# Kernel optimization log

Measured on AMD Instinct MI355X. Metric: run time of the kernel, lower is better.

The kernel has to match this reference:

```python
import jax, jax.numpy as jnp
import numpy as np

RATIO = 2          # BigVGAN Activation1d up/down ratio
K_FILT = 12        # int(6 * ratio // 2) * 2
DILATIONS = (1, 3, 5)


def _kaiser_sinc_filter1d(cutoff, half_width, kernel_size):
    # Faithful port of BigVGAN's kaiser_sinc_filter1d (even kernel path).
    half_size = kernel_size // 2
    delta_f = 4.0 * half_width
    A = 2.285 * (half_size - 1) * np.pi * delta_f + 7.95
    if A > 50.0:
        beta = 0.1102 * (A - 8.7)
    elif A >= 21.0:
        beta = 0.5842 * (A - 21.0) ** 0.4 + 0.07886 * (A - 21.0)
    else:
        beta = 0.0
    window = np.kaiser(kernel_size, beta)              # periodic=False
    time = np.arange(-half_size, half_size) + 0.5       # even kernel size
    filt = 2.0 * cutoff * window * np.sinc(2.0 * cutoff * time)
    filt = filt / filt.sum()
    return jnp.asarray(filt, dtype=jnp.float32)

FILT = _kaiser_sinc_filter1d(0.5 / RATIO, 0.6 / RATIO, K_FILT)


def _depthwise1d(x, filt, stride, lhs_dilation, padding):
    # x: (B, T, C), filt: (k,) shared across channels (depthwise)
    C = x.shape[-1]
    kern = jnp.tile(filt[:, None, None], (1, 1, C))  # (k, 1, C)
    return jax.lax.conv_general_dilated(
        x, kern, window_strides=(stride,), padding=padding,
        lhs_dilation=(lhs_dilation,), feature_group_count=C,
        dimension_numbers=('NLC', 'LIO', 'NLC'))


def upsample2(x):
    # BigVGAN UpSample1d(ratio=2): replicate pad -> conv_transpose -> crop
    pad = K_FILT // RATIO - 1                       # 5
    pad_left = pad * RATIO + (K_FILT - RATIO) // 2  # 15
    pad_right = pad * RATIO + (K_FILT - RATIO + 1) // 2  # 15
    x = jnp.pad(x, ((0, 0), (pad, pad), (0, 0)), mode='edge')
    # conv_transpose(stride=r) == lhs-dilated conv with full padding
    # (filter is symmetric, so no flip needed)
    y = RATIO * _depthwise1d(x, FILT, 1, RATIO, [(K_FILT - 1, K_FILT - 1)])
    return y[:, pad_left:-pad_right, :]  # (B, 2T, C)


def downsample2(x):
    # BigVGAN DownSample1d(ratio=2) == LowPassFilter1d(stride=2)
    pad_left = K_FILT // 2 - 1  # 5 (even kernel)
    pad_right = K_FILT // 2     # 6
    x = jnp.pad(x, ((0, 0), (pad_left, pad_right), (0, 0)), mode='edge')
    return _depthwise1d(x, FILT, RATIO, 1, 'VALID')  # (B, T, C)


def snake(x, log_alpha):
    # alpha_logscale=True: alpha = exp(param); x + (1/alpha) sin^2(alpha x)
    alpha = jnp.exp(log_alpha)  # (C,), broadcasts over (B, T, C)
    return x + (1.0 / (alpha + 1e-9)) * jnp.square(jnp.sin(alpha * x))


def act1d(x, log_alpha):
    return downsample2(snake(upsample2(x), log_alpha))


def wn_conv(x, v, g, b, dilation):
    # weight-norm: kernel = v / ||v||_(0,1) * g, then SAME dilated conv
    norm = jnp.linalg.norm(v, axis=(0, 1))[None, None, :]  # (1,1,Cout)
    kern = (v / norm) * g  # (k, Cin, Cout)
    y = jax.lax.conv_general_dilated(
        x, kern, window_strides=(1,), padding='SAME',
        rhs_dilation=(dilation,), dimension_numbers=('NLC', 'LIO', 'NLC'))
    return y + b


def setup_inputs() -> dict:
    key = jax.random.key(0)
    ks = jax.random.split(key, 7)
    B, T, C, K = 4, 8192, 512, 3
    n = len(DILATIONS)
    x = jax.random.normal(ks[0], (B, T, C), dtype=jnp.float32)
    v1 = jax.random.normal(ks[1], (n, K, C, C), dtype=jnp.float32)
    g1 = jax.random.uniform(ks[2], (n, 1, 1, C), dtype=jnp.float32)
    b1 = 0.01 * jax.random.normal(ks[3], (n, C), dtype=jnp.float32)
    v2 = jax.random.normal(ks[4], (n, K, C, C), dtype=jnp.float32)
    g2 = jax.random.uniform(ks[5], (n, 1, 1, C), dtype=jnp.float32)
    b2 = 0.01 * jax.random.normal(ks[6], (n, C), dtype=jnp.float32)
    alphas = jnp.zeros((2 * n, C), dtype=jnp.float32)  # log-alpha init 0
    return {'x': x, 'v1': v1, 'g1': g1, 'b1': b1,
            'v2': v2, 'g2': g2, 'b2': b2, 'alphas': alphas}


def reference(x, v1, g1, b1, v2, g2, b2, alphas):
    for i, d in enumerate(DILATIONS):
        xt = act1d(x, alphas[2 * i])
        xt = wn_conv(xt, v1[i], g1[i], b1[i], d)
        xt = act1d(xt, alphas[2 * i + 1])
        xt = wn_conv(xt, v2[i], g2[i], b2[i], 1)
        x = xt + x
    return x
```

## Files before the change

kernel.cpp:

```cpp
#include <hip/hip_runtime.h>
#include <math.h>

#define TLEN   8192
#define CCH    512
#define NBATCH 4
#define GUARD_B 8
#define GUARD_T 16
#define XROWS  (TLEN + GUARD_B + GUARD_T)

typedef __attribute__((ext_vector_type(8))) short short8;
typedef __attribute__((ext_vector_type(4))) float f32x4;

struct Filt { float f[12]; };

#define MFMA16(a, b, c) __builtin_amdgcn_mfma_f32_16x16x32_bf16(a, b, c, 0, 0, 0)
#define VMCNT(n)  asm volatile("s_waitcnt vmcnt(" #n ")" ::: "memory")

__device__ __forceinline__ unsigned short f2bf(float f) {
  unsigned u = __float_as_uint(f);
  unsigned r = (u + 0x7fffu + ((u >> 16) & 1u)) >> 16;
  return (unsigned short)r;
}

__device__ __forceinline__ float bf2f(unsigned short u) {
  return __uint_as_float((unsigned)u << 16);
}

__device__ __forceinline__ float fast_sin(float x) {
  float r = x * 0.15915494309189535f;
  r -= floorf(r);
  return __builtin_amdgcn_sinf(r);
}

__device__ __forceinline__ float snake1(float u, float a, float rcp) {
  float s = fast_sin(a * u);
  return fmaf(rcp * s, s, u);
}

__device__ __forceinline__ void gload16(const void* g, void* l) {
  __builtin_amdgcn_global_load_lds(
      (const __attribute__((address_space(1))) unsigned int*)g,
      (__attribute__((address_space(3))) unsigned int*)l, 16, 0, 0);
}

__global__ __launch_bounds__(256)
void normp_k(const float* __restrict__ v1, const float* __restrict__ v2,
             float* __restrict__ part) {
  __shared__ float red[256];
  const int c  = blockIdx.x;
  const int cc = blockIdx.y;
  const int jc = blockIdx.z;
  const int col = threadIdx.x & 63;
  const int js  = threadIdx.x >> 6;
  const int co = cc * 64 + col;
  const float* v = (c < 3) ? v1 + (size_t)c * 3 * CCH * CCH
                           : v2 + (size_t)(c - 3) * 3 * CCH * CCH;
  const int j0 = jc * 64 + js * 16;
  float s = 0.f;
  #pragma unroll
  for (int jj = 0; jj < 16; ++jj) {
    float w = v[(size_t)(j0 + jj) * CCH + co];
    s = fmaf(w, w, s);
  }
  red[threadIdx.x] = s;
  __syncthreads();
  if (threadIdx.x < 64) {
    float t = red[threadIdx.x] + red[threadIdx.x + 64] +
              red[threadIdx.x + 128] + red[threadIdx.x + 192];
    part[(size_t)(c * CCH + co) * 24 + jc] = t;
  }
}

__global__ __launch_bounds__(256)
void fin_k(const float* __restrict__ part, const float* __restrict__ g1,
           const float* __restrict__ g2, float* __restrict__ scl) {
  const int i = blockIdx.x * 256 + threadIdx.x;
  const int c = i >> 9, co = i & 511;
  float s = 0.f;
  #pragma unroll
  for (int jc = 0; jc < 24; ++jc) s += part[(size_t)i * 24 + jc];
  const float g = (c < 3) ? g1[c * CCH + co] : g2[(c - 3) * CCH + co];
  scl[i] = g / sqrtf(s);
}

__global__ __launch_bounds__(512)
void zguard_k(unsigned short* __restrict__ xb) {
  const int b = blockIdx.x / 24;
  const int g = blockIdx.x % 24;
  const int row = (g < 8) ? g : (TLEN + g);
  xb[((size_t)b * XROWS + row) * CCH + threadIdx.x] = 0;
}

__global__ __launch_bounds__(256)
void wprep_k(const float* __restrict__ v1, const float* __restrict__ v2,
             const float* __restrict__ scl, unsigned short* __restrict__ wp) {
  const int gtid = blockIdx.x * 256 + threadIdx.x;
  const int lane = gtid & 63;
  const int gw = gtid >> 6;
  const int c  = gw / 1536;
  const int r  = gw - c * 1536;
  const int s  = r >> 5;
  const int r2 = r & 31;
  const int g8 = r2 >> 2;
  const int j  = r2 & 3;
  const int tap = s % 3, c16 = s / 3;
  const int co  = g8 * 64 + j * 16 + (lane & 15);
  const int ci0 = c16 * 32 + (lane >> 4) * 8;
  const float* v = (c < 3) ? v1 + (size_t)c * 3 * CCH * CCH
                           : v2 + (size_t)(c - 3) * 3 * CCH * CCH;
  const float sc = scl[c * CCH + co];
  unsigned short o[8];
  #pragma unroll
  for (int jj = 0; jj < 8; ++jj) {
    float w = v[((size_t)tap * CCH + ci0 + jj) * CCH + co] * sc;
    o[jj] = f2bf(w);
  }
  *reinterpret_cast<short8*>(wp + (size_t)gw * 512 + lane * 8) =
      *reinterpret_cast<const short8*>(o);
}

template<int INBF>
__global__ __launch_bounds__(256)
void act_k(const void* __restrict__ xin, unsigned short* __restrict__ y,
           const float* __restrict__ la, Filt F) {
  const int idx = blockIdx.x * 256 + threadIdx.x;
  const int c  = (idx & 127) << 2;
  const int ts = (idx >> 7) & 2047;
  const int b  = idx >> 18;
  const int t0 = ts * 4;

  auto ldrow = [&](int row) -> f32x4 {
    if constexpr (INBF) {
      const unsigned short* p =
          (const unsigned short*)xin + ((size_t)b * TLEN + row) * CCH + c;
      ushort4 u = *reinterpret_cast<const ushort4*>(p);
      f32x4 r;
      r[0] = bf2f(u.x); r[1] = bf2f(u.y); r[2] = bf2f(u.z); r[3] = bf2f(u.w);
      return r;
    } else {
      const float* p = (const float*)xin + ((size_t)b * TLEN + row) * CCH + c;
      return *reinterpret_cast<const f32x4*>(p);
    }
  };

  float av[4], rv[4];
  #pragma unroll
  for (int ch = 0; ch < 4; ++ch) {
    av[ch] = expf(la[c + ch]);
    rv[ch] = 1.f / (av[ch] + 1e-9f);
  }

  float acc[4][4];

  if (ts >= 2 && ts <= 2045) {
    f32x4 xw[14];
    #pragma unroll
    for (int j = 0; j < 14; ++j) xw[j] = ldrow(t0 - 5 + j);

    #pragma unroll
    for (int ch = 0; ch < 4; ++ch) {
      float s[18];
      #pragma unroll
      for (int mi = 0; mi < 18; ++mi) {
        float u = 0.f;
        if (mi & 1) {
          const int base = (mi - 5) / 2 + 2;
          #pragma unroll
          for (int r = 0; r < 6; ++r) u = fmaf(F.f[2*r], xw[base + r][ch], u);
        } else {
          const int base = (mi - 6) / 2 + 3;
          #pragma unroll
          for (int r = 0; r < 6; ++r) u = fmaf(F.f[2*r+1], xw[base + r][ch], u);
        }
        u *= 2.f;
        s[mi] = snake1(u, av[ch], rv[ch]);
      }
      #pragma unroll
      for (int tt = 0; tt < 4; ++tt) {
        float a = 0.f;
        #pragma unroll
        for (int k = 0; k < 12; ++k) a = fmaf(F.f[k], s[2*tt + k], a);
        acc[tt][ch] = a;
      }
    }
  } else {
    #pragma unroll
    for (int tt = 0; tt < 4; ++tt) {
      const int t = t0 + tt;
      float a0=0.f, a1=0.f, a2=0.f, a3=0.f;
      for (int k = 0; k < 12; ++k) {
        int m  = 2*t + k - 5;
        int mc = m < 0 ? 0 : (m > 2*TLEN - 1 ? 2*TLEN - 1 : m);
        int tp = mc >> 1;
        int odd = mc & 1;
        float u0=0.f,u1=0.f,u2=0.f,u3=0.f;
        #pragma unroll
        for (int r = 0; r < 6; ++r) {
          int i  = odd ? (tp + r - 2) : (tp + r - 3);
          int ic = i < 0 ? 0 : (i > TLEN - 1 ? TLEN - 1 : i);
          float tap = odd ? F.f[2*r+1] : F.f[2*r];
          f32x4 xv = ldrow(ic);
          u0 = fmaf(tap, xv[0], u0); u1 = fmaf(tap, xv[1], u1);
          u2 = fmaf(tap, xv[2], u2); u3 = fmaf(tap, xv[3], u3);
        }
        u0 *= 2.f; u1 *= 2.f; u2 *= 2.f; u3 *= 2.f;
        const float fk = F.f[k];
        a0 = fmaf(fk, snake1(u0,av[0],rv[0]), a0);
        a1 = fmaf(fk, snake1(u1,av[1],rv[1]), a1);
        a2 = fmaf(fk, snake1(u2,av[2],rv[2]), a2);
        a3 = fmaf(fk, snake1(u3,av[3],rv[3]), a3);
      }
      acc[tt][0]=a0; acc[tt][1]=a1; acc[tt][2]=a2; acc[tt][3]=a3;
    }
  }

  #pragma unroll
  for (int tt = 0; tt < 4; ++tt) {
    ushort4 o;
    o.x = f2bf(acc[tt][0]); o.y = f2bf(acc[tt][1]);
    o.z = f2bf(acc[tt][2]); o.w = f2bf(acc[tt][3]);
    *reinterpret_cast<ushort4*>(
        y + ((size_t)b * XROWS + GUARD_B + t0 + tt) * CCH + c) = o;
  }
}

template<int DIL, int MODE>
__global__ __launch_bounds__(256, 2)
void convm_k(const unsigned short* __restrict__ xb,
             const unsigned short* __restrict__ wp,
             const float* __restrict__ bia,
             const float* __restrict__ resf,
             const unsigned short* __restrict__ resb,
             float* __restrict__ outf,
             unsigned short* __restrict__ outb) {
  __shared__ unsigned short Abuf[4][2][140 * 32];

  const int tid  = threadIdx.x;
  const int lane = tid & 63;
  const int w    = tid >> 6;
  const int wr   = w >> 1;
  const int wc   = w & 1;

  const int l   = (blockIdx.x & 7) * 64 + (blockIdx.x >> 3);
  const int coB = l & 3;
  const int tb  = l >> 2;
  const int b   = tb >> 5;
  const int t0w = (tb & 31) * 256 + wr * 128;
  const int co0 = coB * 128 + wc * 64;
  const int g8  = coB * 2 + wc;

  const int qq = lane >> 4;
  const int r0 = lane & 15;
  const int a_r = lane >> 2;
  const int a_c = lane & 3;

  const unsigned short* xw0 =
      xb + ((size_t)b * XROWS + GUARD_B + t0w - 6) * CCH;
  unsigned short* const As0 = &Abuf[w][0][0];
  unsigned short* const As1 = &Abuf[w][1][0];

  f32x4 acc[8][4] = {};

  auto stA = [&](int c16, unsigned short* dst) {
    #pragma unroll
    for (int i = 0; i < 9; ++i) {
      const int rb = (i < 8) ? 16 * i : 124;
      const int R  = rb + a_r;
      const int sc = a_c ^ ((R >> 1) & 3);
      gload16(xw0 + (size_t)R * CCH + c16 * 32 + sc * 8, dst + rb * 32);
    }
  };

  stA(0, As0);

  for (int c16 = 0; c16 < 16; ++c16) {
    VMCNT(0);
    const unsigned short* Ab = (c16 & 1) ? As1 : As0;
    if (c16 < 15) stA(c16 + 1, (c16 & 1) ? As0 : As1);

    #pragma unroll
    for (int tap = 0; tap < 3; ++tap) {
      const int s = c16 * 3 + tap;
      const unsigned short* wb =
          wp + (((size_t)s * 8 + g8) * 4) * 512 + lane * 8;
      short8 bf[4];
      #pragma unroll
      for (int j = 0; j < 4; ++j)
        bf[j] = *reinterpret_cast<const short8*>(wb + (size_t)j * 512);

      const int rbase = 6 + (tap - 1) * DIL;
      short8 af[8];
      #pragma unroll
      for (int i = 0; i < 8; ++i) {
        const int row = rbase + i * 16 + r0;
        af[i] = *reinterpret_cast<const short8*>(
            Ab + row * 32 + (qq ^ ((row >> 1) & 3)) * 8);
      }
      __builtin_amdgcn_s_setprio(1);
      #pragma unroll
      for (int i = 0; i < 8; ++i)
        #pragma unroll
        for (int j = 0; j < 4; ++j)
          acc[i][j] = MFMA16(af[i], bf[j], acc[i][j]);
      __builtin_amdgcn_s_setprio(0);
    }
  }

  #pragma unroll
  for (int j = 0; j < 4; ++j) {
    const int co = co0 + j * 16 + r0;
    const float bv = bia[co];
    #pragma unroll
    for (int i = 0; i < 8; ++i) {
      const int t = t0w + i * 16 + qq * 4;
      #pragma unroll
      for (int e = 0; e < 4; ++e) {
        const size_t off = ((size_t)b * TLEN + t + e) * CCH + co;
        float o = acc[i][j][e] + bv;
        if constexpr (MODE == 1) o += resf[off];
        if constexpr (MODE == 2 || MODE == 3) o += bf2f(resb[off]);
        if constexpr (MODE == 3) outf[off] = o;
        else                     outb[off] = f2bf(o);
      }
    }
  }
}

static double bessel_i0(double x) {
  double t = 1.0, s = 1.0, q = x * x * 0.25;
  for (int k = 1; k < 64; ++k) {
    t *= q / ((double)k * (double)k);
    s += t;
    if (t < 1e-18 * s) break;
  }
  return s;
}

static void make_filter(Filt* F) {
  const double cutoff = 0.25, hw = 0.3;
  const int ks = 12, half = 6;
  const double A = 2.285 * (half - 1) * M_PI * (4.0 * hw) + 7.95;
  double beta;
  if (A > 50.0)       beta = 0.1102 * (A - 8.7);
  else if (A >= 21.0) beta = 0.5842 * pow(A - 21.0, 0.4) + 0.07886 * (A - 21.0);
  else                beta = 0.0;
  const double i0b = bessel_i0(beta);
  double f[12], sum = 0.0;
  for (int n = 0; n < 12; ++n) {
    double rr = 2.0 * n / (ks - 1) - 1.0;
    double w  = bessel_i0(beta * sqrt(fmax(0.0, 1.0 - rr * rr))) / i0b;
    double tm = (double)(n - half) + 0.5;
    double sx = 2.0 * cutoff * tm;
    double snc = (sx == 0.0) ? 1.0 : sin(M_PI * sx) / (M_PI * sx);
    f[n] = 2.0 * cutoff * w * snc;
    sum += f[n];
  }
  for (int n = 0; n < 12; ++n) F->f[n] = (float)(f[n] / sum);
}

extern "C" void kernel_launch(void* const* d_in, const int* in_sizes, int n_in,
                              void* d_out, int out_size, void* d_ws, size_t ws_size,
                              hipStream_t stream) {
  (void)in_sizes; (void)n_in; (void)out_size; (void)ws_size;
  const float* x  = (const float*)d_in[0];
  const float* v1 = (const float*)d_in[1];
  const float* g1 = (const float*)d_in[2];
  const float* b1 = (const float*)d_in[3];
  const float* v2 = (const float*)d_in[4];
  const float* g2 = (const float*)d_in[5];
  const float* b2 = (const float*)d_in[6];
  const float* al = (const float*)d_in[7];
  float* out = (float*)d_out;

  const size_t N = (size_t)NBATCH * TLEN * CCH;
  unsigned short* wb1  = (unsigned short*)d_ws;
  unsigned short* xbuf = wb1 + N;
  unsigned short* xres = xbuf + (size_t)NBATCH * XROWS * CCH;
  unsigned short* wp   = xres + N;
  float* part = (float*)(wp + (size_t)6 * 3 * CCH * CCH);
  float* scl  = part + (size_t)6 * CCH * 24;

  Filt F;
  make_filter(&F);

  zguard_k<<<96, 512, 0, stream>>>(xbuf);
  normp_k<<<dim3(6, 8, 24), 256, 0, stream>>>(v1, v2, part);
  fin_k<<<12, 256, 0, stream>>>(part, g1, g2, scl);
  wprep_k<<<2304, 256, 0, stream>>>(v1, v2, scl, wp);

  const int cgrid = NBATCH * (TLEN / 256) * 4;
  const int nblk_act = (NBATCH * 2048 * 128) / 256;
  const size_t wsz = (size_t)3 * CCH * CCH;

  act_k<0><<<nblk_act, 256, 0, stream>>>(x, xbuf, al + 0 * CCH, F);
  convm_k<1, 0><<<cgrid, 256, 0, stream>>>(xbuf, wp + 0 * wsz, b1 + 0 * CCH,
                                           nullptr, nullptr, nullptr, wb1);
  act_k<1><<<nblk_act, 256, 0, stream>>>(wb1, xbuf, al + 1 * CCH, F);
  convm_k<1, 1><<<cgrid, 256, 0, stream>>>(xbuf, wp + 3 * wsz, b2 + 0 * CCH,
                                           x, nullptr, nullptr, xres);

  act_k<1><<<nblk_act, 256, 0, stream>>>(xres, xbuf, al + 2 * CCH, F);
  convm_k<3, 0><<<cgrid, 256, 0, stream>>>(xbuf, wp + 1 * wsz, b1 + 1 * CCH,
                                           nullptr, nullptr, nullptr, wb1);
  act_k<1><<<nblk_act, 256, 0, stream>>>(wb1, xbuf, al + 3 * CCH, F);
  convm_k<1, 2><<<cgrid, 256, 0, stream>>>(xbuf, wp + 4 * wsz, b2 + 1 * CCH,
                                           nullptr, xres, nullptr, xres);

  act_k<1><<<nblk_act, 256, 0, stream>>>(xres, xbuf, al + 4 * CCH, F);
  convm_k<5, 0><<<cgrid, 256, 0, stream>>>(xbuf, wp + 2 * wsz, b1 + 2 * CCH,
                                           nullptr, nullptr, nullptr, wb1);
  act_k<1><<<nblk_act, 256, 0, stream>>>(wb1, xbuf, al + 5 * CCH, F);
  convm_k<1, 3><<<cgrid, 256, 0, stream>>>(xbuf, wp + 5 * wsz, b2 + 2 * CCH,
                                           nullptr, xres, out, nullptr);
}
```

Baseline: 651.6 us.

## Restructure conv GEMM to full-channel tiles with shared LDS weights and channel-blocked input

The activation buffer moves to a channel-blocked layout (16 panels of 32 channels, each time-contiguous), so one 32-channel slab of a time tile is a single contiguous load. The conv kernel now uses 512-thread blocks that each cover 128 timesteps by all 512 output channels. Weights are staged through double-buffered shared memory and shared by all waves, instead of every wave reading them straight from global memory. This reduces redundant weight and input traffic, but adds a block-wide barrier per tap step, uses more shared memory, and holds larger per-wave accumulators that may lower occupancy.

```diff
diff --git a/kernel.cpp b/kernel.cpp
--- a/kernel.cpp
+++ b/kernel.cpp
@@ -14,7 +14,6 @@
 struct Filt { float f[12]; };
 
 #define MFMA16(a, b, c) __builtin_amdgcn_mfma_f32_16x16x32_bf16(a, b, c, 0, 0, 0)
-#define VMCNT(n)  asm volatile("s_waitcnt vmcnt(" #n ")" ::: "memory")
 
 __device__ __forceinline__ unsigned short f2bf(float f) {
   unsigned u = __float_as_uint(f);
@@ -88,7 +87,9 @@
   const int b = blockIdx.x / 24;
   const int g = blockIdx.x % 24;
   const int row = (g < 8) ? g : (TLEN + g);
-  xb[((size_t)b * XROWS + row) * CCH + threadIdx.x] = 0;
+  const int cb = threadIdx.x >> 5;
+  const int ci = threadIdx.x & 31;
+  xb[(((size_t)(b * 16 + cb) * XROWS) + row) * 32 + ci] = 0;
 }
 
 __global__ __launch_bounds__(256)
@@ -100,12 +101,10 @@
   const int c  = gw / 1536;
   const int r  = gw - c * 1536;
   const int s  = r >> 5;
-  const int r2 = r & 31;
-  const int g8 = r2 >> 2;
-  const int j  = r2 & 3;
-  const int tap = s % 3, c16 = s / 3;
-  const int co  = g8 * 64 + j * 16 + (lane & 15);
-  const int ci0 = c16 * 32 + (lane >> 4) * 8;
+  const int chunk = r & 31;
+  const int tap = s % 3, cb32 = s / 3;
+  const int co  = chunk * 16 + (lane & 15);
+  const int ci0 = cb32 * 32 + (lane >> 4) * 8;
   const float* v = (c < 3) ? v1 + (size_t)c * 3 * CCH * CCH
                            : v2 + (size_t)(c - 3) * 3 * CCH * CCH;
   const float sc = scl[c * CCH + co];
@@ -214,18 +213,21 @@
     }
   }
 
+  const int cb = c >> 5;
+  const int cw = c & 31;
+  unsigned short* yb =
+      y + (((size_t)(b * 16 + cb) * XROWS) + GUARD_B + t0) * 32 + cw;
   #pragma unroll
   for (int tt = 0; tt < 4; ++tt) {
     ushort4 o;
     o.x = f2bf(acc[tt][0]); o.y = f2bf(acc[tt][1]);
     o.z = f2bf(acc[tt][2]); o.w = f2bf(acc[tt][3]);
-    *reinterpret_cast<ushort4*>(
-        y + ((size_t)b * XROWS + GUARD_B + t0 + tt) * CCH + c) = o;
+    *reinterpret_cast<ushort4*>(yb + (size_t)tt * 32) = o;
   }
 }
 
 template<int DIL, int MODE>
-__global__ __launch_bounds__(256, 2)
+__global__ __launch_bounds__(512)
 void convm_k(const unsigned short* __restrict__ xb,
              const unsigned short* __restrict__ wp,
              const float* __restrict__ bia,
@@ -233,90 +235,100 @@
              const unsigned short* __restrict__ resb,
              float* __restrict__ outf,
              unsigned short* __restrict__ outb) {
-  __shared__ unsigned short Abuf[4][2][140 * 32];
+  __shared__ unsigned short Abuf[2][144 * 32];
+  __shared__ unsigned short Bbuf[2][32 * 512];
 
   const int tid  = threadIdx.x;
   const int lane = tid & 63;
-  const int w    = tid >> 6;
-  const int wr   = w >> 1;
-  const int wc   = w & 1;
-
-  const int l   = (blockIdx.x & 7) * 64 + (blockIdx.x >> 3);
-  const int coB = l & 3;
-  const int tb  = l >> 2;
-  const int b   = tb >> 5;
-  const int t0w = (tb & 31) * 256 + wr * 128;
-  const int co0 = coB * 128 + wc * 64;
-  const int g8  = coB * 2 + wc;
+  const int wid  = tid >> 6;
+  const int wm   = wid >> 2;
+  const int wn   = wid & 3;
+
+  const int tb = blockIdx.x;
+  const int b  = tb >> 6;
+  const int t0 = (tb & 63) * 128;
 
   const int qq = lane >> 4;
   const int r0 = lane & 15;
-  const int a_r = lane >> 2;
-  const int a_c = lane & 3;
-
-  const unsigned short* xw0 =
-      xb + ((size_t)b * XROWS + GUARD_B + t0w - 6) * CCH;
-  unsigned short* const As0 = &Abuf[w][0][0];
-  unsigned short* const As1 = &Abuf[w][1][0];
-
-  f32x4 acc[8][4] = {};
-
-  auto stA = [&](int c16, unsigned short* dst) {
-    #pragma unroll
-    for (int i = 0; i < 9; ++i) {
-      const int rb = (i < 8) ? 16 * i : 124;
-      const int R  = rb + a_r;
-      const int sc = a_c ^ ((R >> 1) & 3);
-      gload16(xw0 + (size_t)R * CCH + c16 * 32 + sc * 8, dst + rb * 32);
+
+  const unsigned short* xpan = xb + (size_t)b * 16 * XROWS * 32;
+  const unsigned short* wpc  = wp;
+
+  f32x4 acc[4][8] = {};
+
+  auto stA = [&](int cb, int buf) {
+    const unsigned short* base =
+        xpan + ((size_t)cb * XROWS + GUARD_B + t0 - 5) * 32;
+    const int rr = lane >> 2;
+    const int sc = (lane & 3) ^ (rr & 3);
+    {
+      const int i = wid;
+      gload16(base + (size_t)(i * 16 + rr) * 32 + sc * 8,
+              &Abuf[buf][i * 512]);
+    }
+    if (wid == 0) {
+      const int i = 8;
+      gload16(base + (size_t)(i * 16 + rr) * 32 + sc * 8,
+              &Abuf[buf][i * 512]);
     }
   };
-
-  stA(0, As0);
-
-  for (int c16 = 0; c16 < 16; ++c16) {
-    VMCNT(0);
-    const unsigned short* Ab = (c16 & 1) ? As1 : As0;
-    if (c16 < 15) stA(c16 + 1, (c16 & 1) ? As0 : As1);
-
+  auto stB = [&](int s, int buf) {
+    #pragma unroll
+    for (int u = 0; u < 4; ++u) {
+      const int chunk = u * 8 + wid;
+      gload16(wpc + ((size_t)s * 32 + chunk) * 512 + lane * 8,
+              &Bbuf[buf][chunk * 512]);
+    }
+  };
+
+  stA(0, 0);
+  stB(0, 0);
+  __syncthreads();
+
+  for (int cb = 0; cb < 16; ++cb) {
+    const int abuf = cb & 1;
     #pragma unroll
     for (int tap = 0; tap < 3; ++tap) {
-      const int s = c16 * 3 + tap;
-      const unsigned short* wb =
-          wp + (((size_t)s * 8 + g8) * 4) * 512 + lane * 8;
-      short8 bf[4];
-      #pragma unroll
-      for (int j = 0; j < 4; ++j)
-        bf[j] = *reinterpret_cast<const short8*>(wb + (size_t)j * 512);
-
-      const int rbase = 6 + (tap - 1) * DIL;
-      short8 af[8];
-      #pragma unroll
-      for (int i = 0; i < 8; ++i) {
-        const int row = rbase + i * 16 + r0;
-        af[i] = *reinterpret_cast<const short8*>(
-            Ab + row * 32 + (qq ^ ((row >> 1) & 3)) * 8);
+      const int s = cb * 3 + tap;
+      if (s < 47) stB(s + 1, (s + 1) & 1);
+      if (tap == 2 && cb < 15) stA(cb + 1, (cb + 1) & 1);
+
+      short8 bf[8];
+      #pragma unroll
+      for (int j = 0; j < 8; ++j)
+        bf[j] = *reinterpret_cast<const short8*>(
+            &Bbuf[s & 1][(wn * 8 + j) * 512 + lane * 8]);
+      short8 af[4];
+      const int rbase = 5 + (tap - 1) * DIL + wm * 64;
+      #pragma unroll
+      for (int rt = 0; rt < 4; ++rt) {
+        const int row = rbase + rt * 16 + r0;
+        af[rt] = *reinterpret_cast<const short8*>(
+            &Abuf[abuf][row * 32 + (qq ^ (row & 3)) * 8]);
       }
       __builtin_amdgcn_s_setprio(1);
       #pragma unroll
-      for (int i = 0; i < 8; ++i)
+      for (int rt = 0; rt < 4; ++rt)
         #pragma unroll
-        for (int j = 0; j < 4; ++j)
-          acc[i][j] = MFMA16(af[i], bf[j], acc[i][j]);
+        for (int j = 0; j < 8; ++j)
+          acc[rt][j] = MFMA16(af[rt], bf[j], acc[rt][j]);
       __builtin_amdgcn_s_setprio(0);
-    }
-  }
-
-  #pragma unroll
-  for (int j = 0; j < 4; ++j) {
-    const int co = co0 + j * 16 + r0;
+
+      __syncthreads();
+    }
+  }
+
+  #pragma unroll
+  for (int j = 0; j < 8; ++j) {
+    const int co = wn * 128 + j * 16 + r0;
     const float bv = bia[co];
     #pragma unroll
-    for (int i = 0; i < 8; ++i) {
-      const int t = t0w + i * 16 + qq * 4;
+    for (int rt = 0; rt < 4; ++rt) {
+      const int t = t0 + wm * 64 + rt * 16 + qq * 4;
       #pragma unroll
       for (int e = 0; e < 4; ++e) {
         const size_t off = ((size_t)b * TLEN + t + e) * CCH + co;
-        float o = acc[i][j][e] + bv;
+        float o = acc[rt][j][e] + bv;
         if constexpr (MODE == 1) o += resf[off];
         if constexpr (MODE == 2 || MODE == 3) o += bf2f(resb[off]);
         if constexpr (MODE == 3) outf[off] = o;
@@ -375,7 +387,7 @@
   const size_t N = (size_t)NBATCH * TLEN * CCH;
   unsigned short* wb1  = (unsigned short*)d_ws;
   unsigned short* xbuf = wb1 + N;
-  unsigned short* xres = xbuf + (size_t)NBATCH * XROWS * CCH;
+  unsigned short* xres = xbuf + (size_t)NBATCH * 16 * XROWS * 32;
   unsigned short* wp   = xres + N;
   float* part = (float*)(wp + (size_t)6 * 3 * CCH * CCH);
   float* scl  = part + (size_t)6 * CCH * 24;
@@ -388,28 +400,28 @@
   fin_k<<<12, 256, 0, stream>>>(part, g1, g2, scl);
   wprep_k<<<2304, 256, 0, stream>>>(v1, v2, scl, wp);
 
-  const int cgrid = NBATCH * (TLEN / 256) * 4;
+  const int cgrid = NBATCH * (TLEN / 128);
   const int nblk_act = (NBATCH * 2048 * 128) / 256;
   const size_t wsz = (size_t)3 * CCH * CCH;
 
   act_k<0><<<nblk_act, 256, 0, stream>>>(x, xbuf, al + 0 * CCH, F);
-  convm_k<1, 0><<<cgrid, 256, 0, stream>>>(xbuf, wp + 0 * wsz, b1 + 0 * CCH,
+  convm_k<1, 0><<<cgrid, 512, 0, stream>>>(xbuf, wp + 0 * wsz, b1 + 0 * CCH,
                                            nullptr, nullptr, nullptr, wb1);
   act_k<1><<<nblk_act, 256, 0, stream>>>(wb1, xbuf, al + 1 * CCH, F);
-  convm_k<1, 1><<<cgrid, 256, 0, stream>>>(xbuf, wp + 3 * wsz, b2 + 0 * CCH,
+  convm_k<1, 1><<<cgrid, 512, 0, stream>>>(xbuf, wp + 3 * wsz, b2 + 0 * CCH,
                                            x, nullptr, nullptr, xres);
 
   act_k<1><<<nblk_act, 256, 0, stream>>>(xres, xbuf, al + 2 * CCH, F);
-  convm_k<3, 0><<<cgrid, 256, 0, stream>>>(xbuf, wp + 1 * wsz, b1 + 1 * CCH,
+  convm_k<3, 0><<<cgrid, 512, 0, stream>>>(xbuf, wp + 1 * wsz, b1 + 1 * CCH,
                                            nullptr, nullptr, nullptr, wb1);
   act_k<1><<<nblk_act, 256, 0, stream>>>(wb1, xbuf, al + 3 * CCH, F);
-  convm_k<1, 2><<<cgrid, 256, 0, stream>>>(xbuf, wp + 4 * wsz, b2 + 1 * CCH,
+  convm_k<1, 2><<<cgrid, 512, 0, stream>>>(xbuf, wp + 4 * wsz, b2 + 1 * CCH,
                                            nullptr, xres, nullptr, xres);
 
   act_k<1><<<nblk_act, 256, 0, stream>>>(xres, xbuf, al + 4 * CCH, F);
-  convm_k<5, 0><<<cgrid, 256, 0, stream>>>(xbuf, wp + 2 * wsz, b1 + 2 * CCH,
+  convm_k<5, 0><<<cgrid, 512, 0, stream>>>(xbuf, wp + 2 * wsz, b1 + 2 * CCH,
                                            nullptr, nullptr, nullptr, wb1);
   act_k<1><<<nblk_act, 256, 0, stream>>>(wb1, xbuf, al + 5 * CCH, F);
-  convm_k<1, 3><<<cgrid, 256, 0, stream>>>(xbuf, wp + 5 * wsz, b2 + 2 * CCH,
+  convm_k<1, 3><<<cgrid, 512, 0, stream>>>(xbuf, wp + 5 * wsz, b2 + 2 * CCH,
                                            nullptr, xres, out, nullptr);
 }
```

After: 760.7 us. 16.7% more time.
